# Performance work log

Measured on AMD Instinct MI355X. Metric: run time of the kernel, lower is better.

The kernel has to match this reference:

```python
import math
import jax, jax.numpy as jnp
import numpy as np

NUM_HEADS = 16
HIDDEN = 1024
HEAD_SIZE = HIDDEN // NUM_HEADS
B, S = 4, 2048


def setup_inputs() -> dict:
    key = jax.random.key(0)
    k1, k2, k3 = jax.random.split(key, 3)
    scale = 1.0 / math.sqrt(HIDDEN)
    return {
        "hidden_states": jax.random.normal(k1, (B, S, HIDDEN), dtype=jnp.float32),
        "attention_mask": jnp.ones((B, S), dtype=jnp.float32),
        "Wq": jax.random.normal(k2, (HIDDEN, HIDDEN), dtype=jnp.float32) * scale,
        "bq": jnp.zeros((HIDDEN,), dtype=jnp.float32),
        "Wk": jax.random.normal(k3, (HIDDEN, HIDDEN), dtype=jnp.float32) * scale,
        "bk": jnp.zeros((HIDDEN,), dtype=jnp.float32),
    }


def reference(hidden_states, attention_mask, Wq, bq, Wk, bk):
    b, s, _ = hidden_states.shape
    # Linear projections (torch Linear: x @ W.T + b)
    q = hidden_states @ Wq.T + bq  # [B,S,H]
    k = hidden_states @ Wk.T + bk  # [B,S,H]
    # split heads: [B, nH, S, dH]
    q = q.reshape(b, s, NUM_HEADS, HEAD_SIZE).transpose(0, 2, 1, 3)
    k = k.reshape(b, s, NUM_HEADS, HEAD_SIZE).transpose(0, 2, 1, 3)
    scores = jnp.einsum("bhqd,bhkd->bhqk", q, k)  # [B,nH,S,S]
    scores = scores / math.sqrt(HEAD_SIZE)  # sqrtatt=True
    scores = jnp.mean(scores, axis=1)  # aggregation='mean' -> [B,S,S]
    scores = scores * attention_mask[:, None, :]  # mask keys (cols)
    scores = scores * attention_mask[:, :, None]  # mask queries (rows)
    return scores
```

## Files before the change

kernel.cpp:

```cpp
#include <hip/hip_runtime.h>
#include <hip/hip_bf16.h>
#include <stdint.h>

#define S_LEN 2048
#define BATCH 4
#define HID 1024
#define M_ROWS (BATCH * S_LEN)

typedef __attribute__((ext_vector_type(8))) short short8;
typedef __attribute__((ext_vector_type(4))) float f32x4;

__device__ __forceinline__ void gload_lds16(const __hip_bfloat16* g,
                                            __hip_bfloat16* l) {
  __builtin_amdgcn_global_load_lds(
      (const __attribute__((address_space(1))) unsigned int*)g,
      (__attribute__((address_space(3))) unsigned int*)l, 16, 0, 0);
}

template <int N>
__device__ __forceinline__ void wait_vm() {
  if constexpr (N == 0)
    asm volatile("s_waitcnt vmcnt(0)" ::: "memory");
  else if constexpr (N == 2)
    asm volatile("s_waitcnt vmcnt(2)" ::: "memory");
  else
    asm volatile("s_waitcnt vmcnt(4)" ::: "memory");
}

__global__ __launch_bounds__(256) void transpose_convert(
    const float* __restrict__ Wq, const float* __restrict__ Wk,
    __hip_bfloat16* __restrict__ WqT, __hip_bfloat16* __restrict__ WkT) {
  __shared__ float tile[32][33];
  const float* src = blockIdx.z ? Wk : Wq;
  __hip_bfloat16* dst = blockIdx.z ? WkT : WqT;
  const int tx = threadIdx.x & 31, ty = threadIdx.x >> 5;
  const int r0 = blockIdx.y * 32, c0 = blockIdx.x * 32;
#pragma unroll
  for (int rr = 0; rr < 4; ++rr) {
    const int r = ty + rr * 8;
    tile[r][tx] = src[(size_t)(r0 + r) * HID + c0 + tx];
  }
  __syncthreads();
#pragma unroll
  for (int rr = 0; rr < 4; ++rr) {
    const int r = ty + rr * 8;
    dst[(size_t)(c0 + r) * HID + r0 + tx] = __float2bfloat16(tile[tx][r]);
  }
}

__global__ __launch_bounds__(256) void bias_stage1(
    const __hip_bfloat16* __restrict__ WqT,
    const __hip_bfloat16* __restrict__ WkT, const float* __restrict__ bq,
    const float* __restrict__ bk, float* __restrict__ a1,
    float* __restrict__ a2, float* __restrict__ cbuf) {
  const int g = blockIdx.x * 4 + (threadIdx.x >> 6);
  const int l = threadIdx.x & 63;
  const int mat = g & 1;
  const int j = g >> 1;
  const __hip_bfloat16* W = mat ? WkT : WqT;
  const float* bv = mat ? bq : bk;
  float s = 0.f;
#pragma unroll
  for (int e = 0; e < 16; ++e)
    s += __bfloat162float(W[(size_t)j * HID + l * 16 + e]) * bv[l * 16 + e];
#pragma unroll
  for (int m = 1; m < 64; m <<= 1) s += __shfl_xor(s, m, 64);
  if (l == 0) (mat ? a2 : a1)[j] = s;
  if (blockIdx.x == 0 && threadIdx.x < 64) {
    float cs = 0.f;
#pragma unroll
    for (int e = 0; e < 16; ++e)
      cs += bq[threadIdx.x * 16 + e] * bk[threadIdx.x * 16 + e];
#pragma unroll
    for (int m = 1; m < 64; m <<= 1) cs += __shfl_xor(cs, m, 64);
    if (threadIdx.x == 0) cbuf[0] = cs;
  }
}

__global__ __launch_bounds__(256) void convert_hs(
    const float* __restrict__ hs, const float* __restrict__ a1,
    const float* __restrict__ a2, const float* __restrict__ cbuf,
    __hip_bfloat16* __restrict__ hs_bf, float* __restrict__ u,
    float* __restrict__ w) {
  const int i = blockIdx.x;
  const int t = threadIdx.x;
  float4 v = *reinterpret_cast<const float4*>(hs + (size_t)i * HID + t * 4);
  __hip_bfloat16 tmp[4] = {__float2bfloat16(v.x), __float2bfloat16(v.y),
                           __float2bfloat16(v.z), __float2bfloat16(v.w)};
  *reinterpret_cast<ushort4*>(hs_bf + (size_t)i * HID + t * 4) =
      *reinterpret_cast<const ushort4*>(tmp);
  float4 A1 = *reinterpret_cast<const float4*>(a1 + t * 4);
  float4 A2 = *reinterpret_cast<const float4*>(a2 + t * 4);
  float pu = v.x * A1.x + v.y * A1.y + v.z * A1.z + v.w * A1.w;
  float pw = v.x * A2.x + v.y * A2.y + v.z * A2.z + v.w * A2.w;
#pragma unroll
  for (int m = 1; m < 64; m <<= 1) {
    pu += __shfl_xor(pu, m, 64);
    pw += __shfl_xor(pw, m, 64);
  }
  __shared__ float su[4], sw[4];
  if ((t & 63) == 0) { su[t >> 6] = pu; sw[t >> 6] = pw; }
  __syncthreads();
  if (t == 0) {
    u[i] = su[0] + su[1] + su[2] + su[3] + cbuf[0];
    w[i] = sw[0] + sw[1] + sw[2] + sw[3];
  }
}

template <int NT, int NF>
__device__ __forceinline__ void gemm_core(
    const __hip_bfloat16* __restrict__ A, const __hip_bfloat16* __restrict__ B,
    const int lda, const int ldb, __hip_bfloat16* lds, f32x4 acc[8][NF]) {
  constexpr int NH = NF / 2;
  const int t = threadIdx.x;
  const int wid = t >> 6;
  const int l = t & 63;
  const int lr = l & 15;
  const int lk = l >> 4;
  const int wr = wid >> 2;
  const int wc = wid & 3;
  const int trow = t >> 3;
  const int tslot = (t & 7) ^ (trow & 7);
  const int rsx = lr & 7;

  __hip_bfloat16* const A0 = lds;
  __hip_bfloat16* const A1 = lds + 16384;
  __hip_bfloat16* const B0 = lds + 32768;
  __hip_bfloat16* const B1 = B0 + NF * 64 * 64;

  short8 fa[4][2], fb[NF][2];

#define STAGE_U(lb, gb, ld, half, kt) do {                                    \
    gload_lds16((gb) + (size_t)((half)*128 + 0  + trow) * (ld) + (kt)*64 +    \
                    tslot * 8,                                                \
                (lb) + ((half)*128 + 0) * 64 + wid * 512);                    \
    gload_lds16((gb) + (size_t)((half)*128 + 64 + trow) * (ld) + (kt)*64 +    \
                    tslot * 8,                                                \
                (lb) + ((half)*128 + 64) * 64 + wid * 512);                   \
  } while (0)

#define LDA_H(mh, Ac) do {                                                    \
    _Pragma("unroll") for (int m = 0; m < 4; ++m)                             \
    _Pragma("unroll") for (int kk = 0; kk < 2; ++kk)                          \
      fa[m][kk] = *reinterpret_cast<const short8*>(                           \
          (Ac) + (wr * 128 + (mh)*64 + m * 16 + lr) * 64 +                    \
          (((kk * 4 + lk) ^ rsx) * 8));                                       \
  } while (0)

#define LDB_H(nh, Bc) do {                                                    \
    _Pragma("unroll") for (int n = 0; n < NH; ++n)                            \
    _Pragma("unroll") for (int kk = 0; kk < 2; ++kk)                          \
      fb[(nh)*NH + n][kk] = *reinterpret_cast<const short8*>(                 \
          (Bc) + (wc * (NF * 16) + (nh) * (NH * 16) + n * 16 + lr) * 64 +     \
          (((kk * 4 + lk) ^ rsx) * 8));                                       \
  } while (0)

#define MFMA_Q(mh, nh) do {                                                   \
    __builtin_amdgcn_s_setprio(1);                                            \
    _Pragma("unroll") for (int m = 0; m < 4; ++m)                             \
    _Pragma("unroll") for (int n = 0; n < NH; ++n)                            \
    _Pragma("unroll") for (int kk = 0; kk < 2; ++kk)                          \
      acc[(mh)*4 + m][(nh)*NH + n] = __builtin_amdgcn_mfma_f32_16x16x32_bf16( \
          fa[m][kk], fb[(nh)*NH + n][kk], acc[(mh)*4 + m][(nh)*NH + n],       \
          0, 0, 0);                                                           \
    __builtin_amdgcn_s_setprio(0);                                            \
  } while (0)

#define CFENCE asm volatile("" ::: "memory")
#define BAR_PRE do { CFENCE; __builtin_amdgcn_s_barrier();                    \
    asm volatile("s_waitcnt lgkmcnt(0)" ::: "memory"); } while (0)
#define BAR_POST do { CFENCE; __builtin_amdgcn_s_barrier(); CFENCE; } while (0)

  STAGE_U(A0, A, lda, 0, 0); STAGE_U(A0, A, lda, 1, 0);
  STAGE_U(B0, B, ldb, 0, 0); if (NH == 2) STAGE_U(B0, B, ldb, 1, 0);
  STAGE_U(B1, B, ldb, 0, 1); if (NH == 2) STAGE_U(B1, B, ldb, 1, 1);
  wait_vm<2 * NH>();
  __builtin_amdgcn_s_barrier();
  CFENCE;

#pragma unroll 2
  for (int tt = 0; tt < NT; ++tt) {
    const int cur = tt & 1;
    __hip_bfloat16* const Ac = cur ? A1 : A0;
    __hip_bfloat16* const An = cur ? A0 : A1;
    __hip_bfloat16* const Bc = cur ? B1 : B0;
    LDA_H(0, Ac); LDB_H(0, Bc);
    if (tt + 1 < NT) STAGE_U(An, A, lda, 0, tt + 1);
    BAR_PRE; MFMA_Q(0, 0); BAR_POST;
    LDB_H(1, Bc);
    if (tt + 1 < NT) STAGE_U(An, A, lda, 1, tt + 1);
    BAR_PRE; MFMA_Q(0, 1); BAR_POST;
    LDA_H(1, Ac);
    if (tt + 2 < NT) STAGE_U(Bc, B, ldb, 0, tt + 2);
    BAR_PRE; MFMA_Q(1, 1); BAR_POST;
    if (NH == 2 && tt + 2 < NT) STAGE_U(Bc, B, ldb, 1, tt + 2);
    BAR_PRE; MFMA_Q(1, 0);
    if (tt + 2 < NT) wait_vm<2 * NH>(); else wait_vm<0>();
    BAR_POST;
  }
#undef STAGE_U
#undef LDA_H
#undef LDB_H
#undef MFMA_Q
#undef CFENCE
#undef BAR_PRE
#undef BAR_POST
}

__global__ __launch_bounds__(512, 2) void wmid_gemm(
    const __hip_bfloat16* __restrict__ WkT,
    const __hip_bfloat16* __restrict__ WqT, float* __restrict__ part) {
  extern __shared__ char smem[];
  __hip_bfloat16* lds = reinterpret_cast<__hip_bfloat16*>(smem);
  const int kz = blockIdx.z;
  f32x4 acc[8][4];
#pragma unroll
  for (int m = 0; m < 8; ++m)
#pragma unroll
    for (int n = 0; n < 4; ++n) acc[m][n] = (f32x4){0.f, 0.f, 0.f, 0.f};

  gemm_core<4, 4>(WkT + (size_t)blockIdx.y * 256 * HID + kz * 256,
                  WqT + (size_t)blockIdx.x * 256 * HID + kz * 256, HID, HID,
                  lds, acc);

  float* outp = part + (size_t)kz * (HID * HID);
  const int t = threadIdx.x, wid = t >> 6, l = t & 63;
  const int wr = wid >> 2, wcn = wid & 3;
  const int lr = l & 15, lg = l >> 4;
#pragma unroll
  for (int m = 0; m < 8; ++m)
#pragma unroll
    for (int n = 0; n < 4; ++n) {
      const int col = blockIdx.x * 256 + wcn * 64 + n * 16 + lr;
#pragma unroll
      for (int r = 0; r < 4; ++r) {
        const int row = blockIdx.y * 256 + wr * 128 + m * 16 + lg * 4 + r;
        outp[(size_t)row * HID + col] = acc[m][n][r];
      }
    }
}

__global__ __launch_bounds__(256) void wmid_reduce(
    const float* __restrict__ part, __hip_bfloat16* __restrict__ wmid_bf) {
  const int idx = (blockIdx.x * 256 + threadIdx.x) * 4;
  float4 s0 = *reinterpret_cast<const float4*>(part + idx);
  float4 s1 = *reinterpret_cast<const float4*>(part + (HID * HID) + idx);
  float4 s2 = *reinterpret_cast<const float4*>(part + 2 * (HID * HID) + idx);
  float4 s3 = *reinterpret_cast<const float4*>(part + 3 * (HID * HID) + idx);
  __hip_bfloat16 tmp[4] = {__float2bfloat16(s0.x + s1.x + s2.x + s3.x),
                           __float2bfloat16(s0.y + s1.y + s2.y + s3.y),
                           __float2bfloat16(s0.z + s1.z + s2.z + s3.z),
                           __float2bfloat16(s0.w + s1.w + s2.w + s3.w)};
  *reinterpret_cast<ushort4*>(wmid_bf + idx) =
      *reinterpret_cast<const ushort4*>(tmp);
}

__global__ __launch_bounds__(512, 2) void t_gemm(
    const __hip_bfloat16* __restrict__ hs_bf,
    const __hip_bfloat16* __restrict__ wmid_bf,
    __hip_bfloat16* __restrict__ T) {
  extern __shared__ char smem[];
  __hip_bfloat16* lds = reinterpret_cast<__hip_bfloat16*>(smem);
  f32x4 acc[8][2];
#pragma unroll
  for (int m = 0; m < 8; ++m)
#pragma unroll
    for (int n = 0; n < 2; ++n) acc[m][n] = (f32x4){0.f, 0.f, 0.f, 0.f};

  gemm_core<16, 2>(hs_bf + (size_t)blockIdx.y * 256 * HID,
                   wmid_bf + (size_t)blockIdx.x * 128 * HID, HID, HID, lds,
                   acc);

  const int t = threadIdx.x, wid = t >> 6, l = t & 63;
  const int wr = wid >> 2, wcn = wid & 3;
  const int lr = l & 15, lg = l >> 4;
#pragma unroll
  for (int m = 0; m < 8; ++m)
#pragma unroll
    for (int n = 0; n < 2; ++n) {
      const int col = blockIdx.x * 128 + wcn * 32 + n * 16 + lr;
#pragma unroll
      for (int r = 0; r < 4; ++r) {
        const int row = blockIdx.y * 256 + wr * 128 + m * 16 + lg * 4 + r;
        T[(size_t)row * HID + col] = __float2bfloat16(acc[m][n][r]);
      }
    }
}

__global__ __launch_bounds__(512, 2) void scores_gemm(
    const __hip_bfloat16* __restrict__ T, const __hip_bfloat16* __restrict__ hs_bf,
    const float* __restrict__ mask, const float* __restrict__ u,
    const float* __restrict__ w, float* __restrict__ out) {
  extern __shared__ char smem[];
  __hip_bfloat16* lds = reinterpret_cast<__hip_bfloat16*>(smem);
  const int b = blockIdx.z;
  const int bm = blockIdx.y, bn = blockIdx.x;

  f32x4 acc[8][4];
#pragma unroll
  for (int m = 0; m < 8; ++m)
#pragma unroll
    for (int n = 0; n < 4; ++n) acc[m][n] = (f32x4){0.f, 0.f, 0.f, 0.f};

  gemm_core<16, 4>(T + ((size_t)b * S_LEN + bm * 256) * HID,
                   hs_bf + ((size_t)b * S_LEN + bn * 256) * HID, HID, HID,
                   lds, acc);

  const int t = threadIdx.x, wid = t >> 6, l = t & 63;
  const int wr = wid >> 2, wcn = wid & 3;
  const int lr = l & 15, lg = l >> 4;
  const float inv = 1.0f / 128.0f;
#pragma unroll
  for (int m = 0; m < 8; ++m)
#pragma unroll
    for (int n = 0; n < 4; ++n) {
      const int col = bn * 256 + wcn * 64 + n * 16 + lr;
      const float mc = mask[b * S_LEN + col];
      const float wadd = w[b * S_LEN + col];
#pragma unroll
      for (int r = 0; r < 4; ++r) {
        const int row = bm * 256 + wr * 128 + m * 16 + lg * 4 + r;
        const float mr = mask[b * S_LEN + row];
        const float uadd = u[b * S_LEN + row];
        out[(size_t)b * S_LEN * S_LEN + (size_t)row * S_LEN + col] =
            (acc[m][n][r] + uadd + wadd) * inv * mc * mr;
      }
    }
}

extern "C" void kernel_launch(void* const* d_in, const int* in_sizes, int n_in,
                              void* d_out, int out_size, void* d_ws,
                              size_t ws_size, hipStream_t stream) {
  const float* hs   = (const float*)d_in[0];
  const float* mask = (const float*)d_in[1];
  const float* Wq   = (const float*)d_in[2];
  const float* bq   = (const float*)d_in[3];
  const float* Wk   = (const float*)d_in[4];
  const float* bk   = (const float*)d_in[5];
  float* out = (float*)d_out;

  char* ws = (char*)d_ws;
  __hip_bfloat16* hs_bf   = (__hip_bfloat16*)(ws);
  float*          wmid_p  = (float*)(ws + 16777216);
  __hip_bfloat16* T_bf    = (__hip_bfloat16*)(ws + 16777216);
  __hip_bfloat16* WqT     = (__hip_bfloat16*)(ws + 33554432);
  __hip_bfloat16* WkT     = (__hip_bfloat16*)(ws + 35651584);
  __hip_bfloat16* wmid_bf = (__hip_bfloat16*)(ws + 37748736);
  float*          a1      = (float*)(ws + 39845888);
  float*          a2      = (float*)(ws + 39849984);
  float*          cbuf    = (float*)(ws + 39854080);
  float*          uvec    = (float*)(ws + 39858176);
  float*          wvec    = (float*)(ws + 39890944);

  (void)hipFuncSetAttribute((const void*)wmid_gemm,
                            hipFuncAttributeMaxDynamicSharedMemorySize, 131072);
  (void)hipFuncSetAttribute((const void*)t_gemm,
                            hipFuncAttributeMaxDynamicSharedMemorySize, 98304);
  (void)hipFuncSetAttribute((const void*)scores_gemm,
                            hipFuncAttributeMaxDynamicSharedMemorySize, 131072);

  hipLaunchKernelGGL(transpose_convert, dim3(32, 32, 2), dim3(256), 0, stream,
                     Wq, Wk, WqT, WkT);
  hipLaunchKernelGGL(bias_stage1, dim3(512), dim3(256), 0, stream,
                     WqT, WkT, bq, bk, a1, a2, cbuf);
  hipLaunchKernelGGL(convert_hs, dim3(M_ROWS), dim3(256), 0, stream,
                     hs, a1, a2, cbuf, hs_bf, uvec, wvec);
  hipLaunchKernelGGL(wmid_gemm, dim3(4, 4, 4), dim3(512), 131072, stream,
                     WkT, WqT, wmid_p);
  hipLaunchKernelGGL(wmid_reduce, dim3(1024), dim3(256), 0, stream,
                     wmid_p, wmid_bf);
  hipLaunchKernelGGL(t_gemm, dim3(HID / 128, M_ROWS / 256), dim3(512), 98304,
                     stream, hs_bf, wmid_bf, T_bf);
  hipLaunchKernelGGL(scores_gemm, dim3(S_LEN / 256, S_LEN / 256, BATCH),
                     dim3(512), 131072, stream, T_bf, hs_bf, mask, uvec, wvec,
                     out);
}
```

Measured before the change: 105.2 us.

## Swap MFMA operands for row-contiguous float4 stores and remap scores blocks per XCD

Swaps the A/B operands of the MFMA so each lane holds four consecutive columns of one row. That lets the wmid, T and scores epilogues write float4 or ushort4 vectors instead of scalar strided stores. The scores grid is flattened to 1D, and block ids are remapped so blocks on the same XCD share row and column tiles for better L2 reuse. bias_stage1 now reads the fp32 weights directly with coalesced column dot products in a small grid, which could be slow because each thread runs a serial 1024-long loop.

```diff
diff --git a/kernel.cpp b/kernel.cpp
--- a/kernel.cpp
+++ b/kernel.cpp
@@ -49,24 +49,17 @@
 }
 
 __global__ __launch_bounds__(256) void bias_stage1(
-    const __hip_bfloat16* __restrict__ WqT,
-    const __hip_bfloat16* __restrict__ WkT, const float* __restrict__ bq,
-    const float* __restrict__ bk, float* __restrict__ a1,
-    float* __restrict__ a2, float* __restrict__ cbuf) {
-  const int g = blockIdx.x * 4 + (threadIdx.x >> 6);
-  const int l = threadIdx.x & 63;
-  const int mat = g & 1;
-  const int j = g >> 1;
-  const __hip_bfloat16* W = mat ? WkT : WqT;
+    const float* __restrict__ Wq, const float* __restrict__ Wk,
+    const float* __restrict__ bq, const float* __restrict__ bk,
+    float* __restrict__ a1, float* __restrict__ a2, float* __restrict__ cbuf) {
+  const int mat = blockIdx.y;
+  const int j = blockIdx.x * 256 + threadIdx.x;
+  const float* W = mat ? Wk : Wq;
   const float* bv = mat ? bq : bk;
   float s = 0.f;
-#pragma unroll
-  for (int e = 0; e < 16; ++e)
-    s += __bfloat162float(W[(size_t)j * HID + l * 16 + e]) * bv[l * 16 + e];
-#pragma unroll
-  for (int m = 1; m < 64; m <<= 1) s += __shfl_xor(s, m, 64);
-  if (l == 0) (mat ? a2 : a1)[j] = s;
-  if (blockIdx.x == 0 && threadIdx.x < 64) {
+  for (int i = 0; i < HID; ++i) s += W[(size_t)i * HID + j] * bv[i];
+  (mat ? a2 : a1)[j] = s;
+  if (blockIdx.x == 0 && mat == 0 && threadIdx.x < 64) {
     float cs = 0.f;
 #pragma unroll
     for (int e = 0; e < 16; ++e)
@@ -161,7 +154,7 @@
     _Pragma("unroll") for (int n = 0; n < NH; ++n)                            \
     _Pragma("unroll") for (int kk = 0; kk < 2; ++kk)                          \
       acc[(mh)*4 + m][(nh)*NH + n] = __builtin_amdgcn_mfma_f32_16x16x32_bf16( \
-          fa[m][kk], fb[(nh)*NH + n][kk], acc[(mh)*4 + m][(nh)*NH + n],       \
+          fb[(nh)*NH + n][kk], fa[m][kk], acc[(mh)*4 + m][(nh)*NH + n],       \
           0, 0, 0);                                                           \
     __builtin_amdgcn_s_setprio(0);                                            \
   } while (0)
@@ -228,16 +221,16 @@
   const int wr = wid >> 2, wcn = wid & 3;
   const int lr = l & 15, lg = l >> 4;
 #pragma unroll
-  for (int m = 0; m < 8; ++m)
+  for (int m = 0; m < 8; ++m) {
+    const int row = blockIdx.y * 256 + wr * 128 + m * 16 + lr;
 #pragma unroll
     for (int n = 0; n < 4; ++n) {
-      const int col = blockIdx.x * 256 + wcn * 64 + n * 16 + lr;
-#pragma unroll
-      for (int r = 0; r < 4; ++r) {
-        const int row = blockIdx.y * 256 + wr * 128 + m * 16 + lg * 4 + r;
-        outp[(size_t)row * HID + col] = acc[m][n][r];
-      }
+      const int col = blockIdx.x * 256 + wcn * 64 + n * 16 + lg * 4;
+      f32x4 a = acc[m][n];
+      *reinterpret_cast<float4*>(&outp[(size_t)row * HID + col]) =
+          (float4){a[0], a[1], a[2], a[3]};
     }
+  }
 }
 
 __global__ __launch_bounds__(256) void wmid_reduce(
@@ -275,16 +268,18 @@
   const int wr = wid >> 2, wcn = wid & 3;
   const int lr = l & 15, lg = l >> 4;
 #pragma unroll
-  for (int m = 0; m < 8; ++m)
+  for (int m = 0; m < 8; ++m) {
+    const int row = blockIdx.y * 256 + wr * 128 + m * 16 + lr;
 #pragma unroll
     for (int n = 0; n < 2; ++n) {
-      const int col = blockIdx.x * 128 + wcn * 32 + n * 16 + lr;
-#pragma unroll
-      for (int r = 0; r < 4; ++r) {
-        const int row = blockIdx.y * 256 + wr * 128 + m * 16 + lg * 4 + r;
-        T[(size_t)row * HID + col] = __float2bfloat16(acc[m][n][r]);
-      }
+      const int col = blockIdx.x * 128 + wcn * 32 + n * 16 + lg * 4;
+      f32x4 a = acc[m][n];
+      __hip_bfloat16 tmp[4] = {__float2bfloat16(a[0]), __float2bfloat16(a[1]),
+                               __float2bfloat16(a[2]), __float2bfloat16(a[3])};
+      *reinterpret_cast<ushort4*>(&T[(size_t)row * HID + col]) =
+          *reinterpret_cast<const ushort4*>(tmp);
     }
+  }
 }
 
 __global__ __launch_bounds__(512, 2) void scores_gemm(
@@ -293,8 +288,11 @@
     const float* __restrict__ w, float* __restrict__ out) {
   extern __shared__ char smem[];
   __hip_bfloat16* lds = reinterpret_cast<__hip_bfloat16*>(smem);
-  const int b = blockIdx.z;
-  const int bm = blockIdx.y, bn = blockIdx.x;
+  const int bid = blockIdx.x;
+  const int xcd = bid & 7, slot = bid >> 3;
+  const int b = slot >> 3, sub = slot & 7;
+  const int bm = (xcd & 3) * 2 + (sub >> 2);
+  const int bn = (xcd >> 2) * 4 + (sub & 3);
 
   f32x4 acc[8][4];
 #pragma unroll
@@ -311,21 +309,24 @@
   const int lr = l & 15, lg = l >> 4;
   const float inv = 1.0f / 128.0f;
 #pragma unroll
-  for (int m = 0; m < 8; ++m)
+  for (int m = 0; m < 8; ++m) {
+    const int row = bm * 256 + wr * 128 + m * 16 + lr;
+    const float mr = mask[b * S_LEN + row] * inv;
+    const float uadd = u[b * S_LEN + row];
 #pragma unroll
     for (int n = 0; n < 4; ++n) {
-      const int col = bn * 256 + wcn * 64 + n * 16 + lr;
-      const float mc = mask[b * S_LEN + col];
-      const float wadd = w[b * S_LEN + col];
-#pragma unroll
-      for (int r = 0; r < 4; ++r) {
-        const int row = bm * 256 + wr * 128 + m * 16 + lg * 4 + r;
-        const float mr = mask[b * S_LEN + row];
-        const float uadd = u[b * S_LEN + row];
-        out[(size_t)b * S_LEN * S_LEN + (size_t)row * S_LEN + col] =
-            (acc[m][n][r] + uadd + wadd) * inv * mc * mr;
-      }
+      const int col = bn * 256 + wcn * 64 + n * 16 + lg * 4;
+      float4 mcv = *reinterpret_cast<const float4*>(&mask[b * S_LEN + col]);
+      float4 wv = *reinterpret_cast<const float4*>(&w[b * S_LEN + col]);
+      f32x4 a = acc[m][n];
+      float4 o = {(a[0] + uadd + wv.x) * mr * mcv.x,
+                  (a[1] + uadd + wv.y) * mr * mcv.y,
+                  (a[2] + uadd + wv.z) * mr * mcv.z,
+                  (a[3] + uadd + wv.w) * mr * mcv.w};
+      *reinterpret_cast<float4*>(
+          &out[(size_t)b * S_LEN * S_LEN + (size_t)row * S_LEN + col]) = o;
     }
+  }
 }
 
 extern "C" void kernel_launch(void* const* d_in, const int* in_sizes, int n_in,
@@ -359,10 +360,10 @@
   (void)hipFuncSetAttribute((const void*)scores_gemm,
                             hipFuncAttributeMaxDynamicSharedMemorySize, 131072);
 
+  hipLaunchKernelGGL(bias_stage1, dim3(4, 2), dim3(256), 0, stream,
+                     Wq, Wk, bq, bk, a1, a2, cbuf);
   hipLaunchKernelGGL(transpose_convert, dim3(32, 32, 2), dim3(256), 0, stream,
                      Wq, Wk, WqT, WkT);
-  hipLaunchKernelGGL(bias_stage1, dim3(512), dim3(256), 0, stream,
-                     WqT, WkT, bq, bk, a1, a2, cbuf);
   hipLaunchKernelGGL(convert_hs, dim3(M_ROWS), dim3(256), 0, stream,
                      hs, a1, a2, cbuf, hs_bf, uvec, wvec);
   hipLaunchKernelGGL(wmid_gemm, dim3(4, 4, 4), dim3(512), 131072, stream,
@@ -371,7 +372,6 @@
                      wmid_p, wmid_bf);
   hipLaunchKernelGGL(t_gemm, dim3(HID / 128, M_ROWS / 256), dim3(512), 98304,
                      stream, hs_bf, wmid_bf, T_bf);
-  hipLaunchKernelGGL(scores_gemm, dim3(S_LEN / 256, S_LEN / 256, BATCH),
-                     dim3(512), 131072, stream, T_bf, hs_bf, mask, uvec, wvec,
-                     out);
-}
+  hipLaunchKernelGGL(scores_gemm, dim3(256), dim3(512), 131072, stream,
+                     T_bf, hs_bf, mask, uvec, wvec, out);
+}
```

New measurement: 138.9 us. 32.0% more time.
